# Kernel optimization log

Measured on AMD Instinct MI355X. Metric: run time of the kernel, lower is better.

The kernel has to match this reference:

```python
import jax, jax.numpy as jnp
import numpy as np

N_NODES = 100000
IN_DIM = 64
OUT_DIM = 64
N_EDGES = 1600000


def _undirected_self_loops(edge_index, num_nodes):
    """Symmetrize, add self loops, coalesce (dedup+sort) like the torch module.
    edge_index is an integer constant, so we preprocess with numpy (no grads flow here).
    Returns (src, dst, w) where w are symmetric GCN normalization weights.
    """
    ei = np.asarray(edge_index, dtype=np.int64)
    loops = np.arange(num_nodes, dtype=np.int64)
    full_src = np.concatenate([ei[0], ei[1], loops])
    full_dst = np.concatenate([ei[1], ei[0], loops])
    keys = np.unique(full_src * num_nodes + full_dst)  # coalesce, sorted
    src = keys // num_nodes
    dst = keys % num_nodes
    deg = np.bincount(dst, minlength=num_nodes).clip(min=1)
    inv_sqrt = deg.astype(np.float32) ** -0.5
    w = inv_sqrt[src] * inv_sqrt[dst]
    return src, dst, w


def setup_inputs() -> dict:
    key = jax.random.key(0)
    kx, kw, kb, ke = jax.random.split(key, 4)
    x = jax.random.normal(kx, (N_NODES, IN_DIM), dtype=jnp.float32)
    # nn.Linear params: W (out, in), b (out,)
    W = jax.random.normal(kw, (OUT_DIM, IN_DIM), dtype=jnp.float32) / np.sqrt(IN_DIM)
    b = jax.random.normal(kb, (OUT_DIM,), dtype=jnp.float32) * 0.01
    edge_index = jax.random.randint(ke, (2, N_EDGES), 0, N_NODES, dtype=jnp.int64)
    return {"x": x, "edge_index": edge_index, "W": W, "b": b}


def reference(x, edge_index, W, b) -> jnp.ndarray:
    n = x.shape[0]
    src_np, dst_np, w_np = _undirected_self_loops(edge_index, n)
    src = jnp.asarray(src_np)
    dst = jnp.asarray(dst_np)
    w = jnp.asarray(w_np).astype(x.dtype)  # (E',)
    h = x @ W.T + b                         # (N, out_dim)
    msg = h[src] * w[:, None]               # gather + per-edge scale, (E', out_dim)
    out = jnp.zeros_like(h).at[dst].add(msg)  # scatter-add aggregation
    return out
```

## Files before the change

### kernel.cpp

```cpp
#include <hip/hip_runtime.h>
#include <hip/hip_bf16.h>
#include <stdint.h>

#define NN 100000
#define EE 1600000
#define CAP 80
#define NB 782
#define HTS 8192
#define EMPTY 0xFFFFFFFFu
#define BCH 4096
#define GBIN 391
#define PRIV 36
#define GLIN 1563

typedef float fx4 __attribute__((ext_vector_type(4)));

__device__ __forceinline__ unsigned int mix32(unsigned int x){
  x ^= x >> 16; x *= 0x7feb352du;
  x ^= x >> 15; x *= 0x846ca68bu;
  x ^= x >> 16;
  return x;
}

extern "C" __global__ __launch_bounds__(256)
void k_prep(const float* __restrict__ x, const float* __restrict__ W,
            const float* __restrict__ bias, __hip_bfloat16* __restrict__ hb,
            const int* __restrict__ ei, int* __restrict__ gcnt,
            unsigned int* __restrict__ bbuf){
  __shared__ __align__(16) char sm[17920];
  const int tid = threadIdx.x;
  const int bid = blockIdx.x;
  const bool isbin = (bid < GBIN);
  const int sub = isbin ? bid : (bid - GBIN);

  if (!isbin){
    __hip_bfloat16 (*wt)[72] = reinterpret_cast<__hip_bfloat16(*)[72]>(sm);
    __hip_bfloat16 (*xs)[68] = reinterpret_cast<__hip_bfloat16(*)[68]>(sm + 9216);
    const int lane = tid & 63;
    const int wv   = tid >> 6;
    #pragma unroll
    for (int r = 0; r < 16; ++r){
      int i = r*4 + wv;
      wt[i][lane] = __float2bfloat16(W[lane*64 + i]);
    }
    const int nbase = sub * 64;
    #pragma unroll
    for (int r = 0; r < 4; ++r){
      int idx = r*256 + tid;
      int nl  = idx >> 4;
      int c4  = idx & 15;
      int n   = nbase + nl;
      float4 v = make_float4(0.f,0.f,0.f,0.f);
      if (n < NN) v = reinterpret_cast<const float4*>(x)[(size_t)n*16 + c4];
      xs[c4*4+0][nl] = __float2bfloat16(v.x);
      xs[c4*4+1][nl] = __float2bfloat16(v.y);
      xs[c4*4+2][nl] = __float2bfloat16(v.z);
      xs[c4*4+3][nl] = __float2bfloat16(v.w);
    }
    __syncthreads();

    const int og  = tid & 7;
    const int nl0 = (tid >> 3) * 2;
    float acc[2][8];
    #pragma unroll
    for (int t=0;t<2;++t){
      #pragma unroll
      for (int j=0;j<8;++j) acc[t][j]=0.f;
    }
    #pragma unroll 4
    for (int i=0;i<64;++i){
      uint4 wq = *reinterpret_cast<const uint4*>(&wt[i][og*8]);
      float w0 = __uint_as_float(wq.x << 16), w1 = __uint_as_float(wq.x & 0xFFFF0000u);
      float w2 = __uint_as_float(wq.y << 16), w3 = __uint_as_float(wq.y & 0xFFFF0000u);
      float w4 = __uint_as_float(wq.z << 16), w5 = __uint_as_float(wq.z & 0xFFFF0000u);
      float w6 = __uint_as_float(wq.w << 16), w7 = __uint_as_float(wq.w & 0xFFFF0000u);
      unsigned xv = *reinterpret_cast<const unsigned*>(&xs[i][nl0]);
      float x0 = __uint_as_float(xv << 16);
      float x1 = __uint_as_float(xv & 0xFFFF0000u);
      acc[0][0] += x0*w0; acc[0][1] += x0*w1; acc[0][2] += x0*w2; acc[0][3] += x0*w3;
      acc[0][4] += x0*w4; acc[0][5] += x0*w5; acc[0][6] += x0*w6; acc[0][7] += x0*w7;
      acc[1][0] += x1*w0; acc[1][1] += x1*w1; acc[1][2] += x1*w2; acc[1][3] += x1*w3;
      acc[1][4] += x1*w4; acc[1][5] += x1*w5; acc[1][6] += x1*w6; acc[1][7] += x1*w7;
    }
    float4 b0 = reinterpret_cast<const float4*>(bias)[og*2];
    float4 b1 = reinterpret_cast<const float4*>(bias)[og*2+1];
    float bb[8] = {b0.x,b0.y,b0.z,b0.w,b1.x,b1.y,b1.z,b1.w};
    #pragma unroll
    for (int t=0;t<2;++t){
      int n = nbase + nl0 + t;
      if (n < NN){
        union { uint4 u4; __hip_bfloat16 v[8]; } pk;
        #pragma unroll
        for (int j=0;j<8;++j) pk.v[j] = __float2bfloat16(acc[t][j] + bb[j]);
        reinterpret_cast<uint4*>(&hb[(size_t)n*64])[og] = pk.u4;
      }
    }
  } else {
    int* bcur = reinterpret_cast<int*>(sm);
    for (int i = tid; i < NB; i += 256) bcur[i] = 0;
    __syncthreads();
    const int base4 = sub * (BCH >> 2);
    const int4* ea4 = reinterpret_cast<const int4*>(ei);
    const int4* ec4 = reinterpret_cast<const int4*>(ei + EE);
    #pragma unroll
    for (int r = 0; r < 4; ++r){
      int idx = base4 + r*256 + tid;
      if (idx < (EE >> 2)){
        int4 A = ea4[idx], C = ec4[idx];
#define BIN1(a,c) { \
        int b1 = (c) >> 7, b2 = (a) >> 7; \
        int p1 = atomicAdd(&bcur[b1], 1); \
        int p2 = atomicAdd(&bcur[b2], 1); \
        if (p1 < PRIV) bbuf[((size_t)b1*GBIN + sub)*PRIV + p1] = ((unsigned)(a) << 7) | (unsigned)((c) & 127); \
        if (p2 < PRIV) bbuf[((size_t)b2*GBIN + sub)*PRIV + p2] = ((unsigned)(c) << 7) | (unsigned)((a) & 127); }
        BIN1(A.x, C.x) BIN1(A.y, C.y) BIN1(A.z, C.z) BIN1(A.w, C.w)
#undef BIN1
      }
    }
    __syncthreads();
    for (int bk = tid; bk < NB; bk += 256){
      int c = bcur[bk];
      gcnt[bk*GBIN + sub] = (c < PRIV) ? c : PRIV;
    }
  }
}

extern "C" __global__ __launch_bounds__(256)
void k_dedup(const int* __restrict__ gcnt, const unsigned int* __restrict__ bbuf,
             unsigned int* __restrict__ srclist, int* __restrict__ cnt,
             float* __restrict__ inv){
  __shared__ unsigned int HT[HTS];
  __shared__ int dcur[128];
  __shared__ int scnt[GBIN];
  const int tid = threadIdx.x;
  const int b   = blockIdx.x;
  const int d0  = b << 7;
  uint4* HT4 = reinterpret_cast<uint4*>(HT);
  #pragma unroll
  for (int r = 0; r < 8; ++r) HT4[r*256 + tid] = make_uint4(EMPTY,EMPTY,EMPTY,EMPTY);
  if (tid < 128) dcur[tid] = 0;
  for (int i = tid; i < GBIN; i += 256) scnt[i] = gcnt[b*GBIN + i];
  __syncthreads();

  const unsigned int* base = bbuf + (size_t)b * GBIN * PRIV;
  for (int i = tid; i < GBIN*PRIV; i += 256){
    int seg = i / PRIV;
    int k   = i - seg*PRIV;
    if (k < scnt[seg]){
      unsigned int pk  = base[i];
      unsigned int idx = mix32(pk) & (HTS-1);
      for (;;){
        unsigned int prev = atomicCAS(&HT[idx], EMPTY, pk);
        if (prev == EMPTY || prev == pk) break;
        idx = (idx + 1) & (HTS-1);
      }
    }
  }
  if (tid < 128 && d0 + tid < NN){
    unsigned int pk  = ((unsigned)(d0 + tid) << 7) | (unsigned)tid;
    unsigned int idx = mix32(pk) & (HTS-1);
    for (;;){
      unsigned int prev = atomicCAS(&HT[idx], EMPTY, pk);
      if (prev == EMPTY || prev == pk) break;
      idx = (idx + 1) & (HTS-1);
    }
  }
  __syncthreads();

  for (int i = tid; i < HTS; i += 256){
    unsigned int v = HT[i];
    if (v != EMPTY){
      int dl  = v & 127;
      int pos = atomicAdd(&dcur[dl], 1);
      if (pos < CAP) srclist[(size_t)(d0 + dl) * CAP + pos] = v >> 7;
    }
  }
  __syncthreads();
  if (tid < 128 && d0 + tid < NN){
    int c = dcur[tid];
    cnt[d0 + tid] = c;
    inv[d0 + tid] = rsqrtf((float)c);
  }
}

extern "C" __global__ __launch_bounds__(256)
void k_agg(const __hip_bfloat16* __restrict__ hb, const float* __restrict__ inv,
           const int* __restrict__ cnt, const unsigned int* __restrict__ srclist,
           float* __restrict__ out){
  __shared__ uint2 sv[4][CAP];
  const int wv   = threadIdx.x >> 6;
  const int lane = threadIdx.x & 63;
  const int g    = lane >> 4;
  const int pl   = lane & 15;
  const int d    = blockIdx.x*4 + wv;
  if (d >= NN) return;
  const unsigned int* reg = srclist + (size_t)d * CAP;
  int c = cnt[d]; if (c > CAP) c = CAP;
  const int cp = (c + 15) & ~15;

  if (lane < c){
    unsigned s = __builtin_nontemporal_load(reg + lane);
    sv[wv][lane] = make_uint2(s, __float_as_uint(inv[s]));
  }
  if (64 + lane < c){
    unsigned s = __builtin_nontemporal_load(reg + 64 + lane);
    sv[wv][64 + lane] = make_uint2(s, __float_as_uint(inv[s]));
  }
  { int p = c + lane; if (p < cp) sv[wv][p] = make_uint2(0u, 0u); }

  const char* hbase = (const char*)hb;
  const int   boff  = pl << 3;
  float4 acc[4];
  #pragma unroll
  for (int u=0;u<4;++u) acc[u] = make_float4(0.f,0.f,0.f,0.f);
  #pragma unroll 2
  for (int j = 0; j < cp; j += 16){
    #pragma unroll
    for (int u = 0; u < 4; ++u){
      uint2 e = sv[wv][j + 4*u + g];
      float w = __uint_as_float(e.y);
      uint2 hv = *reinterpret_cast<const uint2*>(hbase + ((size_t)e.x << 7) + boff);
      acc[u].x += w * __uint_as_float(hv.x << 16);
      acc[u].y += w * __uint_as_float(hv.x & 0xFFFF0000u);
      acc[u].z += w * __uint_as_float(hv.y << 16);
      acc[u].w += w * __uint_as_float(hv.y & 0xFFFF0000u);
    }
  }
  float4 r;
  r.x = (acc[0].x+acc[1].x)+(acc[2].x+acc[3].x);
  r.y = (acc[0].y+acc[1].y)+(acc[2].y+acc[3].y);
  r.z = (acc[0].z+acc[1].z)+(acc[2].z+acc[3].z);
  r.w = (acc[0].w+acc[1].w)+(acc[2].w+acc[3].w);
  r.x += __shfl_xor(r.x, 16); r.y += __shfl_xor(r.y, 16);
  r.z += __shfl_xor(r.z, 16); r.w += __shfl_xor(r.w, 16);
  r.x += __shfl_xor(r.x, 32); r.y += __shfl_xor(r.y, 32);
  r.z += __shfl_xor(r.z, 32); r.w += __shfl_xor(r.w, 32);
  if (g == 0){
    float iv = inv[d];
    fx4 o; o.x = r.x*iv; o.y = r.y*iv; o.z = r.z*iv; o.w = r.w*iv;
    __builtin_nontemporal_store(o, reinterpret_cast<fx4*>(&out[(size_t)d*64]) + pl);
  }
}

extern "C" void kernel_launch(void* const* d_in, const int* in_sizes, int n_in,
                              void* d_out, int out_size, void* d_ws, size_t ws_size,
                              hipStream_t stream){
  (void)in_sizes; (void)n_in; (void)out_size; (void)ws_size;
  const float* x  = (const float*)d_in[0];
  const int*   ei = (const int*)  d_in[1];
  const float* W  = (const float*)d_in[2];
  const float* b  = (const float*)d_in[3];
  float* out = (float*)d_out;

  char* ws = (char*)d_ws;
  __hip_bfloat16* hb      = (__hip_bfloat16*)ws;
  float*          inv     = (float*)(ws + 12800000);
  int*            cnt     = (int*)  (ws + 13200000);
  unsigned int*   srclist = (unsigned int*)(ws + 13600000);
  int*            gcnt    = (int*)  (ws + 45600000);
  unsigned int*   bbuf    = (unsigned int*)(ws + 46823168);

  k_prep  <<<GBIN + GLIN, 256, 0, stream>>>(x, W, b, hb, ei, gcnt, bbuf);
  k_dedup <<<NB, 256, 0, stream>>>(gcnt, bbuf, srclist, cnt, inv);
  k_agg   <<<(NN + 3)/4, 256, 0, stream>>>(hb, inv, cnt, srclist, out);
}
```

Measured before the change: 167.4 us.

## Replace single-pass edge binning with two-level radix binning and narrow aggregation lanes

Edge binning now runs in two passes. k_prep scatters edges into 61 coarse destination groups with 256-slot private segments, and a new k_bin2 kernel re-bins those into 13 fine 128-node bins per group. The old scheme wrote to 782 sparse bins with small padded 36-entry segments, and this is meant to reduce scattered writes and the padded scanning in k_dedup. The aggregation kernel also switches to 32 lanes per edge with 4-byte loads and 8 accumulators, so fewer cross-lane reductions are needed. The change adds an extra kernel launch and a round trip through an intermediate buffer, and the fixed per-segment caps could overflow on skewed inputs.

```diff
diff --git a/kernel.cpp b/kernel.cpp
--- a/kernel.cpp
+++ b/kernel.cpp
@@ -5,15 +5,20 @@
 #define NN 100000
 #define EE 1600000
 #define CAP 80
-#define NB 782
+#define SBK 1664
+#define NS 61
+#define NF 13
+#define NBF 793
+#define GBIN 391
+#define S1 256
+#define NB2 4
+#define SEGS 98
+#define S2 1536
 #define HTS 8192
 #define EMPTY 0xFFFFFFFFu
-#define BCH 4096
-#define GBIN 391
-#define PRIV 36
 #define GLIN 1563
 
-typedef float fx4 __attribute__((ext_vector_type(4)));
+typedef float fx2 __attribute__((ext_vector_type(2)));
 
 __device__ __forceinline__ unsigned int mix32(unsigned int x){
   x ^= x >> 16; x *= 0x7feb352du;
@@ -25,8 +30,8 @@
 extern "C" __global__ __launch_bounds__(256)
 void k_prep(const float* __restrict__ x, const float* __restrict__ W,
             const float* __restrict__ bias, __hip_bfloat16* __restrict__ hb,
-            const int* __restrict__ ei, int* __restrict__ gcnt,
-            unsigned int* __restrict__ bbuf){
+            const int* __restrict__ ei, int* __restrict__ c1,
+            unsigned int* __restrict__ buf1){
   __shared__ __align__(16) char sm[17920];
   const int tid = threadIdx.x;
   const int bid = blockIdx.x;
@@ -96,10 +101,10 @@
       }
     }
   } else {
-    int* bcur = reinterpret_cast<int*>(sm);
-    for (int i = tid; i < NB; i += 256) bcur[i] = 0;
+    int* lcnt = reinterpret_cast<int*>(sm);
+    for (int i = tid; i < NS; i += 256) lcnt[i] = 0;
     __syncthreads();
-    const int base4 = sub * (BCH >> 2);
+    const int base4 = sub * 1024;
     const int4* ea4 = reinterpret_cast<const int4*>(ei);
     const int4* ec4 = reinterpret_cast<const int4*>(ei + EE);
     #pragma unroll
@@ -108,30 +113,67 @@
       if (idx < (EE >> 2)){
         int4 A = ea4[idx], C = ec4[idx];
 #define BIN1(a,c) { \
-        int b1 = (c) >> 7, b2 = (a) >> 7; \
-        int p1 = atomicAdd(&bcur[b1], 1); \
-        int p2 = atomicAdd(&bcur[b2], 1); \
-        if (p1 < PRIV) bbuf[((size_t)b1*GBIN + sub)*PRIV + p1] = ((unsigned)(a) << 7) | (unsigned)((c) & 127); \
-        if (p2 < PRIV) bbuf[((size_t)b2*GBIN + sub)*PRIV + p2] = ((unsigned)(c) << 7) | (unsigned)((a) & 127); }
+        int g1 = (c) / SBK; int dl1 = (c) - g1*SBK; \
+        int p1 = atomicAdd(&lcnt[g1], 1); \
+        if (p1 < S1) buf1[((size_t)g1*GBIN + sub)*S1 + p1] = ((unsigned)(a) << 11) | (unsigned)dl1; \
+        int g2 = (a) / SBK; int dl2 = (a) - g2*SBK; \
+        int p2 = atomicAdd(&lcnt[g2], 1); \
+        if (p2 < S1) buf1[((size_t)g2*GBIN + sub)*S1 + p2] = ((unsigned)(c) << 11) | (unsigned)dl2; }
         BIN1(A.x, C.x) BIN1(A.y, C.y) BIN1(A.z, C.z) BIN1(A.w, C.w)
 #undef BIN1
       }
     }
     __syncthreads();
-    for (int bk = tid; bk < NB; bk += 256){
-      int c = bcur[bk];
-      gcnt[bk*GBIN + sub] = (c < PRIV) ? c : PRIV;
+    for (int g = tid; g < NS; g += 256){
+      int c = lcnt[g];
+      c1[g*GBIN + sub] = (c < S1) ? c : S1;
     }
   }
 }
 
 extern "C" __global__ __launch_bounds__(256)
-void k_dedup(const int* __restrict__ gcnt, const unsigned int* __restrict__ bbuf,
+void k_bin2(const int* __restrict__ c1, const unsigned int* __restrict__ buf1,
+            int* __restrict__ c2, unsigned int* __restrict__ buf2){
+  __shared__ int scnt[SEGS];
+  __shared__ int lcnt[NF];
+  const int tid = threadIdx.x;
+  const int g   = blockIdx.x / NB2;
+  const int kb  = blockIdx.x % NB2;
+  const int s0  = kb * SEGS;
+  const int se  = (s0 + SEGS < GBIN) ? (s0 + SEGS) : GBIN;
+  const int nseg = se - s0;
+  for (int i = tid; i < nseg; i += 256) scnt[i] = c1[g*GBIN + s0 + i];
+  if (tid < NF) lcnt[tid] = 0;
+  __syncthreads();
+
+  const unsigned int* src = buf1 + ((size_t)g*GBIN + s0)*S1;
+  const int tot = nseg * S1;
+  for (int i = tid; i < tot; i += 256){
+    int seg = i >> 8;
+    int k   = i & 255;
+    if (k < scnt[seg]){
+      unsigned v  = src[i];
+      unsigned dl = v & 2047;
+      unsigned f  = dl >> 7;
+      unsigned e2 = ((v >> 11) << 7) | (dl & 127);
+      int p = atomicAdd(&lcnt[f], 1);
+      if (p < S2) buf2[(((size_t)(g*NF + f))*NB2 + kb)*S2 + p] = e2;
+    }
+  }
+  __syncthreads();
+  if (tid < NF){
+    int c = lcnt[tid];
+    c2[(g*NF + tid)*NB2 + kb] = (c < S2) ? c : S2;
+  }
+}
+
+extern "C" __global__ __launch_bounds__(256)
+void k_dedup(const int* __restrict__ c2, const unsigned int* __restrict__ buf2,
              unsigned int* __restrict__ srclist, int* __restrict__ cnt,
              float* __restrict__ inv){
   __shared__ unsigned int HT[HTS];
   __shared__ int dcur[128];
-  __shared__ int scnt[GBIN];
+  __shared__ int m4[NB2];
   const int tid = threadIdx.x;
   const int b   = blockIdx.x;
   const int d0  = b << 7;
@@ -139,15 +181,15 @@
   #pragma unroll
   for (int r = 0; r < 8; ++r) HT4[r*256 + tid] = make_uint4(EMPTY,EMPTY,EMPTY,EMPTY);
   if (tid < 128) dcur[tid] = 0;
-  for (int i = tid; i < GBIN; i += 256) scnt[i] = gcnt[b*GBIN + i];
-  __syncthreads();
-
-  const unsigned int* base = bbuf + (size_t)b * GBIN * PRIV;
-  for (int i = tid; i < GBIN*PRIV; i += 256){
-    int seg = i / PRIV;
-    int k   = i - seg*PRIV;
-    if (k < scnt[seg]){
-      unsigned int pk  = base[i];
+  if (tid < NB2) m4[tid] = c2[b*NB2 + tid];
+  __syncthreads();
+
+  const unsigned int* bp = buf2 + (size_t)b * NB2 * S2;
+  #pragma unroll
+  for (int k = 0; k < NB2; ++k){
+    int m = m4[k];
+    for (int i = tid; i < m; i += 256){
+      unsigned int pk  = bp[k*S2 + i];
       unsigned int idx = mix32(pk) & (HTS-1);
       for (;;){
         unsigned int prev = atomicCAS(&HT[idx], EMPTY, pk);
@@ -190,13 +232,13 @@
   __shared__ uint2 sv[4][CAP];
   const int wv   = threadIdx.x >> 6;
   const int lane = threadIdx.x & 63;
-  const int g    = lane >> 4;
-  const int pl   = lane & 15;
+  const int half = lane >> 5;
+  const int pl   = lane & 31;
   const int d    = blockIdx.x*4 + wv;
   if (d >= NN) return;
   const unsigned int* reg = srclist + (size_t)d * CAP;
   int c = cnt[d]; if (c > CAP) c = CAP;
-  const int cp = (c + 15) & ~15;
+  const int c16 = (c + 15) & ~15;
 
   if (lane < c){
     unsigned s = __builtin_nontemporal_load(reg + lane);
@@ -206,39 +248,32 @@
     unsigned s = __builtin_nontemporal_load(reg + 64 + lane);
     sv[wv][64 + lane] = make_uint2(s, __float_as_uint(inv[s]));
   }
-  { int p = c + lane; if (p < cp) sv[wv][p] = make_uint2(0u, 0u); }
+  { int p = c + lane; if (p < c16) sv[wv][p] = make_uint2(0u, 0u); }
 
   const char* hbase = (const char*)hb;
-  const int   boff  = pl << 3;
-  float4 acc[4];
+  const int   boff  = pl << 2;
+  float ax[8], ay[8];
   #pragma unroll
-  for (int u=0;u<4;++u) acc[u] = make_float4(0.f,0.f,0.f,0.f);
-  #pragma unroll 2
-  for (int j = 0; j < cp; j += 16){
-    #pragma unroll
-    for (int u = 0; u < 4; ++u){
-      uint2 e = sv[wv][j + 4*u + g];
+  for (int u=0;u<8;++u){ ax[u]=0.f; ay[u]=0.f; }
+  #pragma unroll 1
+  for (int j = 0; j < c16; j += 16){
+    #pragma unroll
+    for (int u = 0; u < 8; ++u){
+      uint2 e = sv[wv][j + 2*u + half];
       float w = __uint_as_float(e.y);
-      uint2 hv = *reinterpret_cast<const uint2*>(hbase + ((size_t)e.x << 7) + boff);
-      acc[u].x += w * __uint_as_float(hv.x << 16);
-      acc[u].y += w * __uint_as_float(hv.x & 0xFFFF0000u);
-      acc[u].z += w * __uint_as_float(hv.y << 16);
-      acc[u].w += w * __uint_as_float(hv.y & 0xFFFF0000u);
-    }
-  }
-  float4 r;
-  r.x = (acc[0].x+acc[1].x)+(acc[2].x+acc[3].x);
-  r.y = (acc[0].y+acc[1].y)+(acc[2].y+acc[3].y);
-  r.z = (acc[0].z+acc[1].z)+(acc[2].z+acc[3].z);
-  r.w = (acc[0].w+acc[1].w)+(acc[2].w+acc[3].w);
-  r.x += __shfl_xor(r.x, 16); r.y += __shfl_xor(r.y, 16);
-  r.z += __shfl_xor(r.z, 16); r.w += __shfl_xor(r.w, 16);
-  r.x += __shfl_xor(r.x, 32); r.y += __shfl_xor(r.y, 32);
-  r.z += __shfl_xor(r.z, 32); r.w += __shfl_xor(r.w, 32);
-  if (g == 0){
+      unsigned hv = *reinterpret_cast<const unsigned*>(hbase + ((size_t)e.x << 7) + boff);
+      ax[u] += w * __uint_as_float(hv << 16);
+      ay[u] += w * __uint_as_float(hv & 0xFFFF0000u);
+    }
+  }
+  float rx = ((ax[0]+ax[1])+(ax[2]+ax[3])) + ((ax[4]+ax[5])+(ax[6]+ax[7]));
+  float ry = ((ay[0]+ay[1])+(ay[2]+ay[3])) + ((ay[4]+ay[5])+(ay[6]+ay[7]));
+  rx += __shfl_xor(rx, 32);
+  ry += __shfl_xor(ry, 32);
+  if (half == 0){
     float iv = inv[d];
-    fx4 o; o.x = r.x*iv; o.y = r.y*iv; o.z = r.z*iv; o.w = r.w*iv;
-    __builtin_nontemporal_store(o, reinterpret_cast<fx4*>(&out[(size_t)d*64]) + pl);
+    fx2 o; o.x = rx * iv; o.y = ry * iv;
+    __builtin_nontemporal_store(o, reinterpret_cast<fx2*>(&out[(size_t)d*64 + (pl << 1)]));
   }
 }
 
@@ -257,10 +292,13 @@
   float*          inv     = (float*)(ws + 12800000);
   int*            cnt     = (int*)  (ws + 13200000);
   unsigned int*   srclist = (unsigned int*)(ws + 13600000);
-  int*            gcnt    = (int*)  (ws + 45600000);
-  unsigned int*   bbuf    = (unsigned int*)(ws + 46823168);
-
-  k_prep  <<<GBIN + GLIN, 256, 0, stream>>>(x, W, b, hb, ei, gcnt, bbuf);
-  k_dedup <<<NB, 256, 0, stream>>>(gcnt, bbuf, srclist, cnt, inv);
+  int*            c1      = (int*)  (ws + 45600000);
+  unsigned int*   buf1    = (unsigned int*)(ws + 45696000);
+  int*            c2      = (int*)  (ws + 70120448);
+  unsigned int*   buf2    = (unsigned int*)(ws + 70133760);
+
+  k_prep  <<<GBIN + GLIN, 256, 0, stream>>>(x, W, b, hb, ei, c1, buf1);
+  k_bin2  <<<NS * NB2, 256, 0, stream>>>(c1, buf1, c2, buf2);
+  k_dedup <<<NBF, 256, 0, stream>>>(c2, buf2, srclist, cnt, inv);
   k_agg   <<<(NN + 3)/4, 256, 0, stream>>>(hb, inv, cnt, srclist, out);
 }
```

New measurement: 171.5 us. 1.02x slower.
